# Optimization experiments

Hardware: AMD Instinct MI355X
Metric: run time of the kernel (lower is better)

The kernel has to match this reference:

```python
import jax, jax.numpy as jnp
import numpy as np


def setup_inputs() -> dict:
    key = jax.random.key(0)
    ks = jax.random.split(key, 4)
    B, S, D, U = 4, 4096, 128, 64
    x = jax.random.normal(ks[0], (B, S, D), dtype=jnp.float32)
    Wq = jax.random.normal(ks[1], (D, U), dtype=jnp.float32) * (1.0 / np.sqrt(D))
    Wk = jax.random.normal(ks[2], (D, U), dtype=jnp.float32) * (1.0 / np.sqrt(D))
    Wv = jax.random.normal(ks[3], (D, U), dtype=jnp.float32) * (1.0 / np.sqrt(D))
    bq = jnp.zeros((U,), dtype=jnp.float32)
    bk = jnp.zeros((U,), dtype=jnp.float32)
    bv = jnp.zeros((U,), dtype=jnp.float32)
    return {"x": x, "Wq": Wq, "bq": bq, "Wk": Wk, "bk": bk, "Wv": Wv, "bv": bv}


def reference(x, Wq, bq, Wk, bk, Wv, bv):
    # Single-head, unscaled, unmasked attention (faithful to the Keras layer).
    q = jnp.einsum("bsd,du->bsu", x, Wq) + bq  # [B,S,U]
    k = jnp.einsum("bsd,du->bsu", x, Wk) + bk  # [B,S,U]
    v = jnp.einsum("bsd,du->bsu", x, Wv) + bv  # [B,S,U]
    scores = jnp.einsum("bsu,btu->bst", q, k)  # [B,S,S], no 1/sqrt(d) scaling
    attn = jax.nn.softmax(scores, axis=-1)
    return jnp.einsum("bst,btu->bsu", attn, v)  # [B,S,U]
```

## Files before the change

kernel.cpp:

```cpp
#include <hip/hip_runtime.h>
#include <hip/hip_fp16.h>
#include <math.h>

#define SEQ   4096
#define DIM   128
#define UDIM  64
#define BATCH 4
#define BS    (BATCH*SEQ)

typedef _Float16 h8 __attribute__((ext_vector_type(8)));
typedef _Float16 h4 __attribute__((ext_vector_type(4)));
typedef _Float16 h2 __attribute__((ext_vector_type(2)));
typedef float    f4 __attribute__((ext_vector_type(4)));

#define MFMA_K32(a,b,c) __builtin_amdgcn_mfma_f32_16x16x32_f16((a),(b),(c),0,0,0)
#define MFMA_K16(a,b,c) __builtin_amdgcn_mfma_f32_16x16x16f16((a),(b),(c),0,0,0)

__device__ __forceinline__ h2 pk2(float a, float b) {
  return __builtin_bit_cast(h2, __builtin_amdgcn_cvt_pkrtz(a, b));
}

__device__ __forceinline__ float fexp2(float x) {
#if __has_builtin(__builtin_amdgcn_exp2f)
  return __builtin_amdgcn_exp2f(x);
#else
  return exp2f(x);
#endif
}

#define WT_STRIDE 272
#define KB_STRIDE 144
#define L2E 1.44269504088896f


__global__ __launch_bounds__(256, 3) void proj_mfma(
    const float* __restrict__ x,
    const float* __restrict__ Wq, const float* __restrict__ bq,
    const float* __restrict__ Wk, const float* __restrict__ bk,
    const float* __restrict__ Wv, const float* __restrict__ bv,
    _Float16* __restrict__ qf, _Float16* __restrict__ kswz, _Float16* __restrict__ vswz)
{
  const int proj = blockIdx.y;
  const float* __restrict__ W    = proj==0 ? Wq : (proj==1 ? Wk : Wv);
  const float* __restrict__ bias = proj==0 ? bq : (proj==1 ? bk : bv);
  const int tid  = threadIdx.x;
  const int lane = tid & 63, wv = tid >> 6;
  const int n = lane & 15, quad = lane >> 4;
  const int r0 = blockIdx.x * 64;

  __shared__ __align__(16) char lds[UDIM * WT_STRIDE];
  __shared__ __align__(16) char kbnc[4 * 16 * KB_STRIDE];

  #pragma unroll
  for (int i = 0; i < 8; ++i) {
    const int idx = i*256 + tid;
    const int nn  = idx & 63;
    const int k4  = (idx >> 6) * 4;
    const float w0 = W[(k4+0)*UDIM + nn];
    const float w1 = W[(k4+1)*UDIM + nn];
    const float w2 = W[(k4+2)*UDIM + nn];
    const float w3 = W[(k4+3)*UDIM + nn];
    int2 wd;
    wd.x = __builtin_bit_cast(int, pk2(w0, w1));
    wd.y = __builtin_bit_cast(int, pk2(w2, w3));
    *(int2*)(lds + nn*WT_STRIDE + k4*2) = wd;
  }
  __syncthreads();

  const int row = r0 + wv*16 + n;
  h8 xa[4];
  #pragma unroll
  for (int ks = 0; ks < 4; ++ks) {
    const float* xp = x + (size_t)row*DIM + ks*32 + quad*8;
    const f4 a = *(const f4*)xp, b = *(const f4*)(xp + 4);
    int4 pkd;
    pkd.x = __builtin_bit_cast(int, pk2(a[0], a[1]));
    pkd.y = __builtin_bit_cast(int, pk2(a[2], a[3]));
    pkd.z = __builtin_bit_cast(int, pk2(b[0], b[1]));
    pkd.w = __builtin_bit_cast(int, pk2(b[2], b[3]));
    xa[ks] = __builtin_bit_cast(h8, pkd);
  }

  f4 acc[4];
  #pragma unroll
  for (int nt = 0; nt < 4; ++nt) acc[nt] = (f4){0.f,0.f,0.f,0.f};

  #pragma unroll
  for (int ks = 0; ks < 4; ++ks)
    #pragma unroll
    for (int nt = 0; nt < 4; ++nt) {
      const h8 wf = *(const h8*)(lds + (nt*16 + n)*WT_STRIDE + (ks*32 + quad*8)*2);
      acc[nt] = MFMA_K32(xa[ks], wf, acc[nt]);
    }

  #pragma unroll
  for (int nt = 0; nt < 4; ++nt) {
    const float bb = bias[nt*16 + n];
    #pragma unroll
    for (int r = 0; r < 4; ++r) acc[nt][r] += bb;
  }

  const int b  = r0 / SEQ;
  const int kb = ((r0 % SEQ) >> 4) + wv;

  if (proj == 0) {
    const int par = lane & 1;
    const unsigned sel = par ? 0x03020706u : 0x05040100u;
    #pragma unroll
    for (int nt = 0; nt < 4; ++nt)
      #pragma unroll
      for (int p = 0; p < 2; ++p) {
        const int r = 2*p;
        unsigned A  = __builtin_bit_cast(unsigned, pk2(acc[nt][r], acc[nt][r+1]));
        unsigned Bs = (unsigned)__builtin_amdgcn_mov_dpp((int)A, 0xB1, 0xF, 0xF, true);
        unsigned w  = __builtin_amdgcn_perm(Bs, A, sel);
        const int orow = r0 + wv*16 + 4*quad + r + par;
        const int ocol = nt*16 + n - par;
        *(unsigned*)((char*)qf + ((size_t)orow*UDIM + ocol)*2) = w;
      }
  } else if (proj == 1) {
    char* base = kbnc + wv*(16*KB_STRIDE);
    #pragma unroll
    for (int nt = 0; nt < 4; ++nt)
      #pragma unroll
      for (int r = 0; r < 4; ++r)
        *(_Float16*)(base + (4*quad + r)*KB_STRIDE + (nt*16 + n)*2) =
            (_Float16)acc[nt][r];
    _Float16* kdst = kswz + (size_t)b*SEQ*UDIM;
    #pragma unroll
    for (int ks = 0; ks < 2; ++ks) {
      const h8 f = *(const h8*)(base + n*KB_STRIDE + ks*64 + quad*16);
      *(h8*)(kdst + ((size_t)(kb*2 + ks)*64 + lane)*8) = f;
    }
  } else {
    _Float16* vdst = vswz + (size_t)b*SEQ*UDIM;
    #pragma unroll
    for (int nt = 0; nt < 4; ++nt) {
      int2 t;
      t.x = __builtin_bit_cast(int, pk2(acc[nt][0], acc[nt][1]));
      t.y = __builtin_bit_cast(int, pk2(acc[nt][2], acc[nt][3]));
      *(int2*)(vdst + ((size_t)(kb*4 + nt)*64 + lane)*4) = t;
    }
  }
}

__global__ __launch_bounds__(64, 4) void flash_attn_t(
    const _Float16* __restrict__ qf, const _Float16* __restrict__ kswz,
    const _Float16* __restrict__ vswz,
    _Float16* __restrict__ opart, float* __restrict__ Mp, float* __restrict__ Lp,
    int nkt)
{
  const int qt = blockIdx.x, b = blockIdx.y, sp = blockIdx.z;
  const _Float16* __restrict__ qb = qf   + (size_t)b*SEQ*UDIM;
  const _Float16* __restrict__ kz = kswz + (size_t)b*SEQ*UDIM;
  const _Float16* __restrict__ vz = vswz + (size_t)b*SEQ*UDIM;

  const int lane = threadIdx.x & 63;
  const int n = lane & 15, quad = lane >> 4;
  const int qbase = qt * 32;

  h8 qB[2][2];
  #pragma unroll
  for (int nt = 0; nt < 2; ++nt)
    #pragma unroll
    for (int ks = 0; ks < 2; ++ks)
      qB[nt][ks] = *(const h8*)(qb + (size_t)(qbase + nt*16 + n)*UDIM + ks*32 + quad*8);

  f4 O[4][2], Ol[2];
  #pragma unroll
  for (int ut = 0; ut < 4; ++ut)
    #pragma unroll
    for (int nt = 0; nt < 2; ++nt) O[ut][nt] = (f4){0.f,0.f,0.f,0.f};
  Ol[0] = (f4){0.f,0.f,0.f,0.f};
  Ol[1] = (f4){0.f,0.f,0.f,0.f};

  float M[2] = {-1e30f, -1e30f};

  h4 ones_a;
  { const _Float16 o = (_Float16)1.0f;
    ones_a[0]=o; ones_a[1]=o; ones_a[2]=o; ones_a[3]=o; }

  for (int t = 0; t < nkt; ++t) {
    const int kb0 = (sp*nkt + t) * 4;

    f4 S[4][2];
    #pragma unroll
    for (int mt = 0; mt < 4; ++mt)
      #pragma unroll
      for (int nt = 0; nt < 2; ++nt) S[mt][nt] = (f4){0.f,0.f,0.f,0.f};

    #pragma unroll
    for (int ks = 0; ks < 2; ++ks) {
      h8 ka[4];
      #pragma unroll
      for (int mt = 0; mt < 4; ++mt)
        ka[mt] = *(const h8*)(kz + ((size_t)((kb0 + mt)*2 + ks)*64 + lane)*8);
      #pragma unroll
      for (int mt = 0; mt < 4; ++mt)
        #pragma unroll
        for (int nt = 0; nt < 2; ++nt)
          S[mt][nt] = MFMA_K32(ka[mt], qB[nt][ks], S[mt][nt]);
    }

    h4 vcur[4], vnext[4];
    #pragma unroll
    for (int ut = 0; ut < 4; ++ut)
      vcur[ut] = *(const h4*)(vz + ((size_t)(kb0*4 + ut)*64 + lane)*4);

    float alpha[2];
    #pragma unroll
    for (int nt = 0; nt < 2; ++nt) {
      float rm = S[0][nt][0];
      #pragma unroll
      for (int mt = 0; mt < 4; ++mt)
        #pragma unroll
        for (int r = 0; r < 4; ++r) rm = fmaxf(rm, S[mt][nt][r]);
      rm = fmaxf(rm, __shfl_xor(rm, 16));
      rm = fmaxf(rm, __shfl_xor(rm, 32));
      const float mo = M[nt];
      const float mn = fmaxf(mo, rm);
      alpha[nt] = fexp2((mo - mn) * L2E);
      const float mnl = mn * L2E;
      #pragma unroll
      for (int mt = 0; mt < 4; ++mt)
        #pragma unroll
        for (int r = 0; r < 4; ++r)
          S[mt][nt][r] = fexp2(fmaf(S[mt][nt][r], L2E, -mnl));
      M[nt] = mn;
      #pragma unroll
      for (int ut = 0; ut < 4; ++ut)
        #pragma unroll
        for (int r = 0; r < 4; ++r) O[ut][nt][r] *= alpha[nt];
      #pragma unroll
      for (int r = 0; r < 4; ++r) Ol[nt][r] *= alpha[nt];
    }

    h4 pB[4][2];
    #pragma unroll
    for (int mt = 0; mt < 4; ++mt)
      #pragma unroll
      for (int nt = 0; nt < 2; ++nt) {
        int2 tt;
        tt.x = __builtin_bit_cast(int, pk2(S[mt][nt][0], S[mt][nt][1]));
        tt.y = __builtin_bit_cast(int, pk2(S[mt][nt][2], S[mt][nt][3]));
        pB[mt][nt] = __builtin_bit_cast(h4, tt);
      }

    #pragma unroll
    for (int mt = 0; mt < 4; ++mt) {
      if (mt < 3) {
        #pragma unroll
        for (int ut = 0; ut < 4; ++ut)
          vnext[ut] = *(const h4*)(vz + ((size_t)((kb0 + mt + 1)*4 + ut)*64 + lane)*4);
      }
      #pragma unroll
      for (int ut = 0; ut < 4; ++ut)
        #pragma unroll
        for (int nt = 0; nt < 2; ++nt)
          O[ut][nt] = MFMA_K16(vcur[ut], pB[mt][nt], O[ut][nt]);
      #pragma unroll
      for (int nt = 0; nt < 2; ++nt)
        Ol[nt] = MFMA_K16(ones_a, pB[mt][nt], Ol[nt]);
      #pragma unroll
      for (int ut = 0; ut < 4; ++ut) vcur[ut] = vnext[ut];
    }
  }

  const size_t rowg = (size_t)sp*BS + (size_t)b*SEQ + qbase;
  #pragma unroll
  for (int nt = 0; nt < 2; ++nt) {
    char* __restrict__ orow = (char*)(opart + (rowg + nt*16 + n)*UDIM);
    #pragma unroll
    for (int ut = 0; ut < 4; ++ut)
      #pragma unroll
      for (int p = 0; p < 2; ++p)
        *(unsigned*)(orow + (ut*16 + quad*4 + 2*p)*2) =
            __builtin_bit_cast(unsigned, pk2(O[ut][nt][2*p], O[ut][nt][2*p+1]));
    if (quad == 0) {
      Mp[rowg + nt*16 + n] = M[nt] * L2E;
      Lp[rowg + nt*16 + n] = Ol[nt][0];
    }
  }
}

__global__ __launch_bounds__(256) void merge_out(
    const _Float16* __restrict__ opart, const float* __restrict__ Mp,
    const float* __restrict__ Lp, float* __restrict__ out, int nsplit)
{
  const int tid = threadIdx.x;
  const int row = blockIdx.x*16 + (tid >> 4);
  const int u4  = (tid & 15) * 4;
  float M = -1e30f;
  for (int s = 0; s < nsplit; ++s) M = fmaxf(M, Mp[(size_t)s*BS + row]);
  f4 num = (f4){0.f,0.f,0.f,0.f};
  float den = 0.f;
  for (int s = 0; s < nsplit; ++s) {
    const float w = fexp2(Mp[(size_t)s*BS + row] - M);
    den += w * Lp[(size_t)s*BS + row];
    const h4 op = *(const h4*)(opart + ((size_t)s*BS + row)*UDIM + u4);
    #pragma unroll
    for (int i = 0; i < 4; ++i) num[i] += w * (float)op[i];
  }
  const float dinv = 1.f / den;
  *(f4*)(out + (size_t)row*UDIM + u4) = num * dinv;
}

extern "C" void kernel_launch(void* const* d_in, const int* in_sizes, int n_in,
                              void* d_out, int out_size, void* d_ws, size_t ws_size,
                              hipStream_t stream) {
  (void)in_sizes; (void)n_in; (void)out_size;
  const float* x  = (const float*)d_in[0];
  const float* Wq = (const float*)d_in[1];
  const float* bq = (const float*)d_in[2];
  const float* Wk = (const float*)d_in[3];
  const float* bk = (const float*)d_in[4];
  const float* Wv = (const float*)d_in[5];
  const float* bv = (const float*)d_in[6];
  float* out = (float*)d_out;

  char* ws = (char*)d_ws;
  const size_t fBytes = (size_t)BS * UDIM * 2;
  auto need = [](int nsp) {
    return (size_t)3*BS*UDIM*2 + (size_t)nsp*BS*4*2 + (size_t)nsp*BS*UDIM*2;
  };
  int nsplit;
  if      (ws_size >= need(8)) nsplit = 8;
  else if (ws_size >= need(4)) nsplit = 4;
  else if (ws_size >= need(2)) nsplit = 2;
  else                         nsplit = 1;

  _Float16* qf   = (_Float16*)(ws);
  _Float16* kswz = (_Float16*)(ws + fBytes);
  _Float16* vswz = (_Float16*)(ws + 2*fBytes);
  float* Mp      = (float*)(ws + 3*fBytes);
  float* Lp      = (float*)(ws + 3*fBytes + (size_t)nsplit*BS*4);
  _Float16* opart = (_Float16*)(ws + 3*fBytes + (size_t)nsplit*BS*8);

  proj_mfma<<<dim3(BS/64, 3), 256, 0, stream>>>(x, Wq, bq, Wk, bk, Wv, bv, qf, kswz, vswz);
  flash_attn_t<<<dim3(SEQ/32, BATCH, nsplit), 64, 0, stream>>>(
      qf, kswz, vswz, opart, Mp, Lp, (SEQ/64)/nsplit);
  merge_out<<<dim3(BS/16), 256, 0, stream>>>(opart, Mp, Lp, out, nsplit);
}
```

Baseline: 127.9 us.

## Fold log2e into Q, repack V, use 4-wave blocks, skip no-op rescales

Q is scaled by log2(e) in the projection, so the attention loop computes exp2(S - m) directly without a per-element multiply. V is stored as 8-half vectors so each lane loads 16 bytes at a time, and K/V pointers are advanced incrementally. The attention kernel now runs 4 waves per block over 128 queries. The O/L rescale is skipped when no row max changed across the wave, and the split count can rise to 16. In exchange, Q is scaled before rounding to fp16, and more splits mean more partial outputs for the merge kernel to read.

Result: faster. 123.0 us (-3.8%).

```diff
diff --git a/kernel.cpp b/kernel.cpp
--- a/kernel.cpp
+++ b/kernel.cpp
@@ -19,7 +19,6 @@
 __device__ __forceinline__ h2 pk2(float a, float b) {
   return __builtin_bit_cast(h2, __builtin_amdgcn_cvt_pkrtz(a, b));
 }
-
 __device__ __forceinline__ float fexp2(float x) {
 #if __has_builtin(__builtin_amdgcn_exp2f)
   return __builtin_amdgcn_exp2f(x);
@@ -104,6 +103,10 @@
   const int kb = ((r0 % SEQ) >> 4) + wv;
 
   if (proj == 0) {
+    #pragma unroll
+    for (int nt = 0; nt < 4; ++nt)
+      #pragma unroll
+      for (int r = 0; r < 4; ++r) acc[nt][r] *= L2E;
     const int par = lane & 1;
     const unsigned sel = par ? 0x03020706u : 0x05040100u;
     #pragma unroll
@@ -135,29 +138,34 @@
   } else {
     _Float16* vdst = vswz + (size_t)b*SEQ*UDIM;
     #pragma unroll
-    for (int nt = 0; nt < 4; ++nt) {
-      int2 t;
-      t.x = __builtin_bit_cast(int, pk2(acc[nt][0], acc[nt][1]));
-      t.y = __builtin_bit_cast(int, pk2(acc[nt][2], acc[nt][3]));
-      *(int2*)(vdst + ((size_t)(kb*4 + nt)*64 + lane)*4) = t;
-    }
-  }
-}
-
-__global__ __launch_bounds__(64, 4) void flash_attn_t(
+    for (int pr = 0; pr < 2; ++pr) {
+      int4 t;
+      t.x = __builtin_bit_cast(int, pk2(acc[2*pr][0],   acc[2*pr][1]));
+      t.y = __builtin_bit_cast(int, pk2(acc[2*pr][2],   acc[2*pr][3]));
+      t.z = __builtin_bit_cast(int, pk2(acc[2*pr+1][0], acc[2*pr+1][1]));
+      t.w = __builtin_bit_cast(int, pk2(acc[2*pr+1][2], acc[2*pr+1][3]));
+      *(int4*)(vdst + ((size_t)(kb*2 + pr)*64 + lane)*8) = t;
+    }
+  }
+}
+
+__global__ __launch_bounds__(256, 4) void flash_attn_t(
     const _Float16* __restrict__ qf, const _Float16* __restrict__ kswz,
     const _Float16* __restrict__ vswz,
     _Float16* __restrict__ opart, float* __restrict__ Mp, float* __restrict__ Lp,
     int nkt)
 {
   const int qt = blockIdx.x, b = blockIdx.y, sp = blockIdx.z;
-  const _Float16* __restrict__ qb = qf   + (size_t)b*SEQ*UDIM;
-  const _Float16* __restrict__ kz = kswz + (size_t)b*SEQ*UDIM;
-  const _Float16* __restrict__ vz = vswz + (size_t)b*SEQ*UDIM;
-
-  const int lane = threadIdx.x & 63;
+  const int tid = threadIdx.x;
+  const int lane = tid & 63, wid = tid >> 6;
   const int n = lane & 15, quad = lane >> 4;
-  const int qbase = qt * 32;
+  const int qbase = qt*128 + wid*32;
+
+  const _Float16* __restrict__ qb = qf + (size_t)b*SEQ*UDIM;
+  const _Float16* kpl = kswz + (size_t)b*SEQ*UDIM + (size_t)sp*nkt*4096 + lane*8;
+  const _Float16* kph = kpl + 2048;
+  const _Float16* vpl = vswz + (size_t)b*SEQ*UDIM + (size_t)sp*nkt*4096 + lane*8;
+  const _Float16* vph = vpl + 2048;
 
   h8 qB[2][2];
   #pragma unroll
@@ -181,65 +189,64 @@
     ones_a[0]=o; ones_a[1]=o; ones_a[2]=o; ones_a[3]=o; }
 
   for (int t = 0; t < nkt; ++t) {
-    const int kb0 = (sp*nkt + t) * 4;
+    h8 ka[4][2];
+    ka[0][0] = *(const h8*)(kpl);        ka[0][1] = *(const h8*)(kpl +  512);
+    ka[1][0] = *(const h8*)(kpl + 1024); ka[1][1] = *(const h8*)(kpl + 1536);
+    ka[2][0] = *(const h8*)(kph);        ka[2][1] = *(const h8*)(kph +  512);
+    ka[3][0] = *(const h8*)(kph + 1024); ka[3][1] = *(const h8*)(kph + 1536);
+
+    h8 vc0 = *(const h8*)(vpl);
+    h8 vc1 = *(const h8*)(vpl + 512);
 
     f4 S[4][2];
     #pragma unroll
     for (int mt = 0; mt < 4; ++mt)
       #pragma unroll
       for (int nt = 0; nt < 2; ++nt) S[mt][nt] = (f4){0.f,0.f,0.f,0.f};
-
-    #pragma unroll
-    for (int ks = 0; ks < 2; ++ks) {
-      h8 ka[4];
+    #pragma unroll
+    for (int ks = 0; ks < 2; ++ks)
       #pragma unroll
       for (int mt = 0; mt < 4; ++mt)
-        ka[mt] = *(const h8*)(kz + ((size_t)((kb0 + mt)*2 + ks)*64 + lane)*8);
-      #pragma unroll
-      for (int mt = 0; mt < 4; ++mt)
         #pragma unroll
         for (int nt = 0; nt < 2; ++nt)
-          S[mt][nt] = MFMA_K32(ka[mt], qB[nt][ks], S[mt][nt]);
-    }
-
-    h4 vcur[4], vnext[4];
-    #pragma unroll
-    for (int ut = 0; ut < 4; ++ut)
-      vcur[ut] = *(const h4*)(vz + ((size_t)(kb0*4 + ut)*64 + lane)*4);
-
-    float alpha[2];
+          S[mt][nt] = MFMA_K32(ka[mt][ks], qB[nt][ks], S[mt][nt]);
+
+    float mn[2];
     #pragma unroll
     for (int nt = 0; nt < 2; ++nt) {
-      float rm = S[0][nt][0];
-      #pragma unroll
-      for (int mt = 0; mt < 4; ++mt)
-        #pragma unroll
-        for (int r = 0; r < 4; ++r) rm = fmaxf(rm, S[mt][nt][r]);
+      float m0 = fmaxf(fmaxf(S[0][nt][0], S[0][nt][1]), fmaxf(S[0][nt][2], S[0][nt][3]));
+      float m1 = fmaxf(fmaxf(S[1][nt][0], S[1][nt][1]), fmaxf(S[1][nt][2], S[1][nt][3]));
+      float m2 = fmaxf(fmaxf(S[2][nt][0], S[2][nt][1]), fmaxf(S[2][nt][2], S[2][nt][3]));
+      float m3 = fmaxf(fmaxf(S[3][nt][0], S[3][nt][1]), fmaxf(S[3][nt][2], S[3][nt][3]));
+      float rm = fmaxf(fmaxf(m0, m1), fmaxf(m2, m3));
       rm = fmaxf(rm, __shfl_xor(rm, 16));
       rm = fmaxf(rm, __shfl_xor(rm, 32));
-      const float mo = M[nt];
-      const float mn = fmaxf(mo, rm);
-      alpha[nt] = fexp2((mo - mn) * L2E);
-      const float mnl = mn * L2E;
-      #pragma unroll
-      for (int mt = 0; mt < 4; ++mt)
+      mn[nt] = fmaxf(M[nt], rm);
+    }
+
+    const bool nochange = (mn[0] == M[0]) && (mn[1] == M[1]);
+    if (!__all(nochange)) {
+      #pragma unroll
+      for (int nt = 0; nt < 2; ++nt) {
+        const float alpha = fexp2(M[nt] - mn[nt]);
+        #pragma unroll
+        for (int ut = 0; ut < 4; ++ut)
+          #pragma unroll
+          for (int r = 0; r < 4; ++r) O[ut][nt][r] *= alpha;
+        #pragma unroll
+        for (int r = 0; r < 4; ++r) Ol[nt][r] *= alpha;
+      }
+    }
+    M[0] = mn[0]; M[1] = mn[1];
+
+    h4 pB[4][2];
+    #pragma unroll
+    for (int mt = 0; mt < 4; ++mt)
+      #pragma unroll
+      for (int nt = 0; nt < 2; ++nt) {
         #pragma unroll
         for (int r = 0; r < 4; ++r)
-          S[mt][nt][r] = fexp2(fmaf(S[mt][nt][r], L2E, -mnl));
-      M[nt] = mn;
-      #pragma unroll
-      for (int ut = 0; ut < 4; ++ut)
-        #pragma unroll
-        for (int r = 0; r < 4; ++r) O[ut][nt][r] *= alpha[nt];
-      #pragma unroll
-      for (int r = 0; r < 4; ++r) Ol[nt][r] *= alpha[nt];
-    }
-
-    h4 pB[4][2];
-    #pragma unroll
-    for (int mt = 0; mt < 4; ++mt)
-      #pragma unroll
-      for (int nt = 0; nt < 2; ++nt) {
+          S[mt][nt][r] = fexp2(S[mt][nt][r] - mn[nt]);
         int2 tt;
         tt.x = __builtin_bit_cast(int, pk2(S[mt][nt][0], S[mt][nt][1]));
         tt.y = __builtin_bit_cast(int, pk2(S[mt][nt][2], S[mt][nt][3]));
@@ -248,22 +255,32 @@
 
     #pragma unroll
     for (int mt = 0; mt < 4; ++mt) {
-      if (mt < 3) {
-        #pragma unroll
-        for (int ut = 0; ut < 4; ++ut)
-          vnext[ut] = *(const h4*)(vz + ((size_t)((kb0 + mt + 1)*4 + ut)*64 + lane)*4);
-      }
+      h8 vn0, vn1;
+      if (mt == 0) { vn0 = *(const h8*)(vpl + 1024); vn1 = *(const h8*)(vpl + 1536); }
+      if (mt == 1) { vn0 = *(const h8*)(vph);        vn1 = *(const h8*)(vph +  512); }
+      if (mt == 2) { vn0 = *(const h8*)(vph + 1024); vn1 = *(const h8*)(vph + 1536); }
+      const int4 vi0 = __builtin_bit_cast(int4, vc0);
+      const int4 vi1 = __builtin_bit_cast(int4, vc1);
+      int2 p01, p23, p45, p67;
+      p01.x = vi0.x; p01.y = vi0.y;  p23.x = vi0.z; p23.y = vi0.w;
+      p45.x = vi1.x; p45.y = vi1.y;  p67.x = vi1.z; p67.y = vi1.w;
+      h4 va[4];
+      va[0] = __builtin_bit_cast(h4, p01);
+      va[1] = __builtin_bit_cast(h4, p23);
+      va[2] = __builtin_bit_cast(h4, p45);
+      va[3] = __builtin_bit_cast(h4, p67);
       #pragma unroll
       for (int ut = 0; ut < 4; ++ut)
         #pragma unroll
         for (int nt = 0; nt < 2; ++nt)
-          O[ut][nt] = MFMA_K16(vcur[ut], pB[mt][nt], O[ut][nt]);
+          O[ut][nt] = MFMA_K16(va[ut], pB[mt][nt], O[ut][nt]);
       #pragma unroll
       for (int nt = 0; nt < 2; ++nt)
         Ol[nt] = MFMA_K16(ones_a, pB[mt][nt], Ol[nt]);
-      #pragma unroll
-      for (int ut = 0; ut < 4; ++ut) vcur[ut] = vnext[ut];
-    }
+      if (mt < 3) { vc0 = vn0; vc1 = vn1; }
+    }
+
+    kpl += 4096; kph += 4096; vpl += 4096; vph += 4096;
   }
 
   const size_t rowg = (size_t)sp*BS + (size_t)b*SEQ + qbase;
@@ -277,7 +294,7 @@
         *(unsigned*)(orow + (ut*16 + quad*4 + 2*p)*2) =
             __builtin_bit_cast(unsigned, pk2(O[ut][nt][2*p], O[ut][nt][2*p+1]));
     if (quad == 0) {
-      Mp[rowg + nt*16 + n] = M[nt] * L2E;
+      Mp[rowg + nt*16 + n] = M[nt];
       Lp[rowg + nt*16 + n] = Ol[nt][0];
     }
   }
@@ -324,10 +341,11 @@
     return (size_t)3*BS*UDIM*2 + (size_t)nsp*BS*4*2 + (size_t)nsp*BS*UDIM*2;
   };
   int nsplit;
-  if      (ws_size >= need(8)) nsplit = 8;
-  else if (ws_size >= need(4)) nsplit = 4;
-  else if (ws_size >= need(2)) nsplit = 2;
-  else                         nsplit = 1;
+  if      (ws_size >= need(16)) nsplit = 16;
+  else if (ws_size >= need(8))  nsplit = 8;
+  else if (ws_size >= need(4))  nsplit = 4;
+  else if (ws_size >= need(2))  nsplit = 2;
+  else                          nsplit = 1;
 
   _Float16* qf   = (_Float16*)(ws);
   _Float16* kswz = (_Float16*)(ws + fBytes);
@@ -337,7 +355,7 @@
   _Float16* opart = (_Float16*)(ws + 3*fBytes + (size_t)nsplit*BS*8);
 
   proj_mfma<<<dim3(BS/64, 3), 256, 0, stream>>>(x, Wq, bq, Wk, bk, Wv, bv, qf, kswz, vswz);
-  flash_attn_t<<<dim3(SEQ/32, BATCH, nsplit), 64, 0, stream>>>(
+  flash_attn_t<<<dim3(SEQ/128, BATCH, nsplit), 256, 0, stream>>>(
       qf, kswz, vswz, opart, Mp, Lp, (SEQ/64)/nsplit);
   merge_out<<<dim3(BS/16), 256, 0, stream>>>(opart, Mp, Lp, out, nsplit);
 }
```
